# Kernel tuning notes

Measured on AMD Instinct MI355X. Metric: run time of the kernel, lower is better.

Reference implementation:

```python
import jax, jax.numpy as jnp
import numpy as np

V, E, H, N, L = 32000, 512, 512, 64, 128


def setup_inputs() -> dict:
    key = jax.random.key(0)
    ks = jax.random.split(key, 16)
    s = 0.02  # init scale
    return {
        "input_ids": jax.random.randint(ks[0], (N,), 0, V),
        "h": jax.random.normal(ks[1], (N, H), jnp.float32),
        "c": jax.random.normal(ks[2], (N, H), jnp.float32),
        "encoder_hiddens": jax.random.normal(ks[3], (N, L, H), jnp.float32),
        "attn_mask": jnp.zeros((N, L), dtype=bool),
        "embed_W": jax.random.normal(ks[4], (V, E), jnp.float32) * s,
        "w_ih": jax.random.normal(ks[5], (4 * H, E), jnp.float32) * s,
        "b_ih": jnp.zeros((4 * H,), jnp.float32),
        "w_hh": jax.random.normal(ks[6], (4 * H, H), jnp.float32) * s,
        "b_hh": jnp.zeros((4 * H,), jnp.float32),
        "attn_Wh": jax.random.normal(ks[7], (H, H), jnp.float32) * s,
        "attn_Ws": jax.random.normal(ks[8], (H, H), jnp.float32) * s,
        "attn_v": jax.random.normal(ks[9], (H,), jnp.float32) * s,
        "h2o_W": jax.random.normal(ks[10], (V, 2 * H), jnp.float32) * s,
        "h2o_b": jnp.zeros((V,), jnp.float32),
    }


def reference(input_ids, h, c, encoder_hiddens, attn_mask, embed_W,
              w_ih, b_ih, w_hh, b_hh, attn_Wh, attn_Ws, attn_v,
              h2o_W, h2o_b):
    # Embedding lookup: (N, E)
    emb = embed_W[input_ids]
    # LSTM cell: fused gate GEMMs, chunk order i, f, g, o (torch chunk(4))
    gates = emb @ w_ih.T + b_ih + h @ w_hh.T + b_hh  # (N, 4H)
    i_g, f_g, g_g, o_g = jnp.split(gates, 4, axis=1)
    c_t = jax.nn.sigmoid(f_g) * c + jax.nn.sigmoid(i_g) * jnp.tanh(g_g)
    h_t = jax.nn.sigmoid(o_g) * jnp.tanh(c_t)  # (N, H)
    # Bahdanau attention: v^T tanh(W_h h_t + W_s enc)
    proj = jnp.tanh((h_t @ attn_Wh.T)[:, None, :] + encoder_hiddens @ attn_Ws.T)  # (N, L, H)
    score = jnp.einsum('nlh,h->nl', proj, attn_v)  # (N, L)
    score = jnp.where(attn_mask, -jnp.inf, score)
    attn_w = jax.nn.softmax(score, axis=1)  # (N, L)
    context = jnp.einsum('nl,nlh->nh', attn_w, encoder_hiddens)  # (N, H)
    # Output projection + log-softmax over vocab
    combined = jnp.concatenate([h_t, context], axis=1)  # (N, 2H)
    out = jax.nn.log_softmax(combined @ h2o_W.T + h2o_b, axis=-1)  # (N, V)
    return out, h_t, c_t
```

## Files before the change

### kernel.cpp

```cpp
#include <hip/hip_runtime.h>
#include <math.h>

#define V 32000
#define E 512
#define H 512
#define N 64
#define L 128
#define NV (N*V)
#define NH (N*H)
#define MTOT (N*L)
#define VT 500

typedef short  s8v  __attribute__((ext_vector_type(8)));
typedef float  f4v  __attribute__((ext_vector_type(4)));

__device__ __forceinline__ float sigf(float x) { return 1.0f / (1.0f + __expf(-x)); }

__device__ __forceinline__ unsigned short f2bf(float f) {
    unsigned int u = __float_as_uint(f);
    unsigned int r = u + 0x7FFFu + ((u >> 16) & 1u);
    return (unsigned short)(r >> 16);
}

__global__ __launch_bounds__(256) void k_gates(
    const int* __restrict__ ids, const float* __restrict__ hprev,
    const float* __restrict__ embW, const float* __restrict__ w_ih,
    const float* __restrict__ w_hh, float* __restrict__ gates_p)
{
    __shared__ __align__(16) float xs[64 * 128];
    const int bx = blockIdx.x;
    const int ks = blockIdx.y;
    const int tid = threadIdx.x;
    const bool emb_part = (ks < 4);
    const int koff = (ks & 3) * 128;

    for (int i = tid; i < 64 * 32; i += 256) {
        int n = i >> 5, kk4 = i & 31;
        float4 x4;
        if (emb_part)
            x4 = ((const float4*)(embW + (size_t)ids[n] * E + koff))[kk4];
        else
            x4 = ((const float4*)(hprev + (size_t)n * H + koff))[kk4];
        ((float4*)xs)[n * 32 + kk4] = x4;
    }
    __syncthreads();

    const int jl = tid & 63;
    const int ng = tid >> 6;
    const int j = bx * 64 + jl;
    const int nb = ng * 16;
    const float* wrow = (emb_part ? w_ih : w_hh) + (size_t)j * 512 + koff;

    float acc[16];
#pragma unroll
    for (int i = 0; i < 16; ++i) acc[i] = 0.f;

    for (int e4 = 0; e4 < 32; ++e4) {
        float4 w4 = ((const float4*)wrow)[e4];
#pragma unroll
        for (int i = 0; i < 16; ++i) {
            float4 x4 = ((const float4*)xs)[(nb + i) * 32 + e4];
            acc[i] += w4.x * x4.x + w4.y * x4.y + w4.z * x4.z + w4.w * x4.w;
        }
    }
#pragma unroll
    for (int i = 0; i < 16; ++i)
        gates_p[(size_t)ks * (64 * 2048) + (size_t)(nb + i) * 2048 + j] = acc[i];
}

__global__ __launch_bounds__(256) void k_lstm_pw(
    const float* __restrict__ gates_p, const float* __restrict__ b_ih,
    const float* __restrict__ b_hh, const float* __restrict__ cprev,
    float* __restrict__ out, unsigned short* __restrict__ xb)
{
    int i = blockIdx.x * 256 + threadIdx.x;
    if (i >= NH) return;
    int n = i >> 9, k = i & 511;
    float g[4];
#pragma unroll
    for (int q = 0; q < 4; ++q) {
        int j = q * 512 + k;
        float s = b_ih[j] + b_hh[j];
#pragma unroll
        for (int ks = 0; ks < 8; ++ks)
            s += gates_p[(size_t)ks * (64 * 2048) + (size_t)n * 2048 + j];
        g[q] = s;
    }
    float ig = sigf(g[0]), fg = sigf(g[1]), gg = tanhf(g[2]), og = sigf(g[3]);
    float ct = fg * cprev[i] + ig * gg;
    float ht = og * tanhf(ct);
    out[NV + i] = ht;
    out[NV + NH + i] = ct;
    xb[(size_t)n * 1024 + k] = f2bf(ht);
}

__global__ __launch_bounds__(256) void k_sproj(
    const float* __restrict__ out, const float* __restrict__ Wh,
    float* __restrict__ sproj)
{
    __shared__ __align__(16) float xs[512];
    int n = blockIdx.x >> 1;
    int h = (blockIdx.x & 1) * 256 + threadIdx.x;
    const float* ht = out + NV + (size_t)n * 512;
    for (int i = threadIdx.x; i < 512; i += 256) xs[i] = ht[i];
    __syncthreads();
    const float* wrow = Wh + (size_t)h * 512;
    float acc = 0.f;
    for (int e4 = 0; e4 < 128; ++e4) {
        float4 w4 = ((const float4*)wrow)[e4];
        float4 x4 = ((const float4*)xs)[e4];
        acc += w4.x * x4.x + w4.y * x4.y + w4.z * x4.z + w4.w * x4.w;
    }
    sproj[(size_t)n * 512 + h] = acc;
}

__global__ __launch_bounds__(256) void k_score_gemm(
    const float* __restrict__ enc, const float* __restrict__ Ws,
    const float* __restrict__ sproj, const float* __restrict__ av,
    float* __restrict__ scorep)
{
    __shared__ __align__(16) short As[64 * 72];
    __shared__ __align__(16) short Bs[64 * 72];
    __shared__ float sred[64];

    const int bm = blockIdx.x, bh = blockIdx.y;
    const int tid = threadIdx.x;
    const int w = tid >> 6, l = tid & 63;
    const int wave_m = (w >> 1) * 32, wave_h = (w & 1) * 32;
    const int lq = l >> 4, lr = l & 15;

    if (tid < 64) sred[tid] = 0.f;

    f4v acc[2][2];
#pragma unroll
    for (int i = 0; i < 2; ++i)
#pragma unroll
        for (int j = 0; j < 2; ++j) acc[i][j] = (f4v)0.f;

    for (int kt = 0; kt < 8; ++kt) {
        __syncthreads();
#pragma unroll
        for (int r = 0; r < 2; ++r) {
            int idx = (r * 256 + tid) * 8;
            int row = idx >> 6, col = idx & 63;
            const float* sa = enc + (size_t)(bm * 64 + row) * 512 + kt * 64 + col;
            const float* sb = Ws  + (size_t)(bh * 64 + row) * 512 + kt * 64 + col;
            float4 a0 = *(const float4*)sa, a1 = *(const float4*)(sa + 4);
            float4 b0 = *(const float4*)sb, b1 = *(const float4*)(sb + 4);
            union { unsigned short u[8]; uint4 q; } pa, pb;
            pa.u[0]=f2bf(a0.x); pa.u[1]=f2bf(a0.y); pa.u[2]=f2bf(a0.z); pa.u[3]=f2bf(a0.w);
            pa.u[4]=f2bf(a1.x); pa.u[5]=f2bf(a1.y); pa.u[6]=f2bf(a1.z); pa.u[7]=f2bf(a1.w);
            pb.u[0]=f2bf(b0.x); pb.u[1]=f2bf(b0.y); pb.u[2]=f2bf(b0.z); pb.u[3]=f2bf(b0.w);
            pb.u[4]=f2bf(b1.x); pb.u[5]=f2bf(b1.y); pb.u[6]=f2bf(b1.z); pb.u[7]=f2bf(b1.w);
            *(uint4*)(As + row * 72 + col) = pa.q;
            *(uint4*)(Bs + row * 72 + col) = pb.q;
        }
        __syncthreads();

#pragma unroll
        for (int ks = 0; ks < 2; ++ks) {
            s8v a_frag[2], b_frag[2];
#pragma unroll
            for (int i = 0; i < 2; ++i)
                a_frag[i] = *(const s8v*)(As + (wave_m + 16 * i + lr) * 72 + ks * 32 + lq * 8);
#pragma unroll
            for (int j = 0; j < 2; ++j)
                b_frag[j] = *(const s8v*)(Bs + (wave_h + 16 * j + lr) * 72 + ks * 32 + lq * 8);
#pragma unroll
            for (int i = 0; i < 2; ++i)
#pragma unroll
                for (int j = 0; j < 2; ++j)
                    acc[i][j] = __builtin_amdgcn_mfma_f32_16x16x32_bf16(
                        a_frag[i], b_frag[j], acc[i][j], 0, 0, 0);
        }
    }
    __syncthreads();

    const int hc0 = bh * 64 + wave_h + lr;
#pragma unroll
    for (int i = 0; i < 2; ++i) {
#pragma unroll
        for (int reg = 0; reg < 4; ++reg) {
            int m_local = wave_m + 16 * i + lq * 4 + reg;
            int m = bm * 64 + m_local;
            int n = m >> 7;
            float p = 0.f;
#pragma unroll
            for (int j = 0; j < 2; ++j) {
                int hc = hc0 + 16 * j;
                float val = acc[i][j][reg] + sproj[(size_t)n * 512 + hc];
                p += tanhf(val) * av[hc];
            }
            p += __shfl_xor(p, 1, 64);
            p += __shfl_xor(p, 2, 64);
            p += __shfl_xor(p, 4, 64);
            p += __shfl_xor(p, 8, 64);
            if (lr == 0) atomicAdd(&sred[m_local], p);
        }
    }
    __syncthreads();
    if (tid < 64)
        scorep[(size_t)bh * MTOT + bm * 64 + tid] = sred[tid];
}

__global__ __launch_bounds__(512) void k_softmax_ctx(
    const float* __restrict__ scorep, const unsigned char* __restrict__ mask,
    const float* __restrict__ enc, unsigned short* __restrict__ xb)
{
    __shared__ float sc[128];
    __shared__ float wl[128];
    const int n = blockIdx.x, t = threadIdx.x;

    if (t < 128) {
        float s = 0.f;
#pragma unroll
        for (int q = 0; q < 8; ++q)
            s += scorep[(size_t)q * MTOT + n * 128 + t];
        if (mask[(size_t)n * 128 + t]) s = -1e30f;
        sc[t] = s;
    }
    __syncthreads();
    if (t < 64) {
        float m = fmaxf(sc[t], sc[t + 64]);
#pragma unroll
        for (int off = 32; off > 0; off >>= 1) m = fmaxf(m, __shfl_xor(m, off, 64));
        float e0 = __expf(sc[t] - m), e1 = __expf(sc[t + 64] - m);
        float ss = e0 + e1;
#pragma unroll
        for (int off = 32; off > 0; off >>= 1) ss += __shfl_xor(ss, off, 64);
        float inv = 1.0f / ss;
        wl[t] = e0 * inv;
        wl[t + 64] = e1 * inv;
    }
    __syncthreads();

    const float* encn = enc + (size_t)n * L * H + t;
    float acc = 0.f;
#pragma unroll 4
    for (int ll = 0; ll < 128; ++ll)
        acc += wl[ll] * encn[(size_t)ll * 512];
    xb[(size_t)n * 1024 + 512 + t] = f2bf(acc);
}

__global__ __launch_bounds__(256) void k_logits(
    const float* __restrict__ h2oW, const unsigned short* __restrict__ xb,
    const float* __restrict__ h2ob, float* __restrict__ dlogits,
    float* __restrict__ pmax, float* __restrict__ psum)
{
    __shared__ __align__(16) short As[64 * 72];
    __shared__ __align__(16) short Bs[64 * 72];
    __shared__ __align__(16) float cs[64 * 68];

    const int bm = blockIdx.x;
    const int tid = threadIdx.x;
    const int w = tid >> 6, l = tid & 63;
    const int wave_m = (w & 1) * 32, wave_n = (w >> 1) * 32;
    const int lq = l >> 4, lr = l & 15;

    const int arow = tid >> 2;
    const int acol = (tid & 3) * 16;
    const float* aptr = h2oW + (size_t)(bm * 64 + arow) * 1024 + acol;
    const unsigned short* bptr = xb + (size_t)arow * 1024 + acol;

    f4v acc[2][2];
#pragma unroll
    for (int i = 0; i < 2; ++i)
#pragma unroll
        for (int j = 0; j < 2; ++j) acc[i][j] = (f4v)0.f;

    float4 ra[4];
    uint4  rb[2];
#pragma unroll
    for (int r = 0; r < 4; ++r) ra[r] = ((const float4*)aptr)[r];
    rb[0] = *(const uint4*)bptr;
    rb[1] = *(const uint4*)(bptr + 8);

#pragma unroll 1
    for (int kt = 0; kt < 16; ++kt) {
        if (kt) __syncthreads();
        union { unsigned short u[8]; uint4 q; } p0, p1;
        p0.u[0]=f2bf(ra[0].x); p0.u[1]=f2bf(ra[0].y); p0.u[2]=f2bf(ra[0].z); p0.u[3]=f2bf(ra[0].w);
        p0.u[4]=f2bf(ra[1].x); p0.u[5]=f2bf(ra[1].y); p0.u[6]=f2bf(ra[1].z); p0.u[7]=f2bf(ra[1].w);
        p1.u[0]=f2bf(ra[2].x); p1.u[1]=f2bf(ra[2].y); p1.u[2]=f2bf(ra[2].z); p1.u[3]=f2bf(ra[2].w);
        p1.u[4]=f2bf(ra[3].x); p1.u[5]=f2bf(ra[3].y); p1.u[6]=f2bf(ra[3].z); p1.u[7]=f2bf(ra[3].w);
        *(uint4*)(As + arow * 72 + acol)     = p0.q;
        *(uint4*)(As + arow * 72 + acol + 8) = p1.q;
        *(uint4*)(Bs + arow * 72 + acol)     = rb[0];
        *(uint4*)(Bs + arow * 72 + acol + 8) = rb[1];
        __syncthreads();

        if (kt < 15) {
            const float* ap = aptr + (kt + 1) * 64;
            const unsigned short* bp = bptr + (kt + 1) * 64;
#pragma unroll
            for (int r = 0; r < 4; ++r) ra[r] = ((const float4*)ap)[r];
            rb[0] = *(const uint4*)bp;
            rb[1] = *(const uint4*)(bp + 8);
        }

#pragma unroll
        for (int ks = 0; ks < 2; ++ks) {
            s8v a_frag[2], b_frag[2];
#pragma unroll
            for (int i = 0; i < 2; ++i)
                a_frag[i] = *(const s8v*)(As + (wave_m + 16 * i + lr) * 72 + ks * 32 + lq * 8);
#pragma unroll
            for (int j = 0; j < 2; ++j)
                b_frag[j] = *(const s8v*)(Bs + (wave_n + 16 * j + lr) * 72 + ks * 32 + lq * 8);
#pragma unroll
            for (int i = 0; i < 2; ++i)
#pragma unroll
                for (int j = 0; j < 2; ++j)
                    acc[i][j] = __builtin_amdgcn_mfma_f32_16x16x32_bf16(
                        a_frag[i], b_frag[j], acc[i][j], 0, 0, 0);
        }
    }
    __syncthreads();

#pragma unroll
    for (int i = 0; i < 2; ++i)
#pragma unroll
        for (int j = 0; j < 2; ++j)
#pragma unroll
            for (int reg = 0; reg < 4; ++reg)
                cs[(wave_n + 16 * j + lr) * 68 + wave_m + 16 * i + lq * 4 + reg] = acc[i][j][reg];
    __syncthreads();

    const int n = tid >> 2, q = tid & 3;
    const int v0 = bm * 64 + q * 16;
    float4 vals[4];
    float m_loc = -1e30f;
#pragma unroll
    for (int k = 0; k < 4; ++k) {
        float4 cv = *(const float4*)(cs + n * 68 + q * 16 + 4 * k);
        float4 bv = *(const float4*)(h2ob + v0 + 4 * k);
        cv.x += bv.x; cv.y += bv.y; cv.z += bv.z; cv.w += bv.w;
        vals[k] = cv;
        *(float4*)(dlogits + (size_t)n * V + v0 + 4 * k) = cv;
        m_loc = fmaxf(m_loc, fmaxf(fmaxf(cv.x, cv.y), fmaxf(cv.z, cv.w)));
    }
    float s_loc = 0.f;
#pragma unroll
    for (int k = 0; k < 4; ++k) {
        s_loc += __expf(vals[k].x - m_loc) + __expf(vals[k].y - m_loc)
               + __expf(vals[k].z - m_loc) + __expf(vals[k].w - m_loc);
    }
    float m2 = fmaxf(m_loc, __shfl_xor(m_loc, 1, 64));
    m2 = fmaxf(m2, __shfl_xor(m2, 2, 64));
    s_loc *= __expf(m_loc - m2);
    float s2 = s_loc + __shfl_xor(s_loc, 1, 64);
    s2 += __shfl_xor(s2, 2, 64);
    if (q == 0) {
        pmax[(size_t)n * VT + bm] = m2;
        psum[(size_t)n * VT + bm] = s2;
    }
}

__global__ __launch_bounds__(256) void k_lse(
    const float* __restrict__ pmax, const float* __restrict__ psum,
    float* __restrict__ lse)
{
    __shared__ float rm[4], rs[4];
    const int n = blockIdx.x, t = threadIdx.x;
    float m0 = (t < VT) ? pmax[(size_t)n * VT + t] : -1e30f;
    float m1 = (t + 256 < VT) ? pmax[(size_t)n * VT + t + 256] : -1e30f;
    float mm = fmaxf(m0, m1);
#pragma unroll
    for (int off = 32; off > 0; off >>= 1) mm = fmaxf(mm, __shfl_xor(mm, off, 64));
    if ((t & 63) == 0) rm[t >> 6] = mm;
    __syncthreads();
    float m = fmaxf(fmaxf(rm[0], rm[1]), fmaxf(rm[2], rm[3]));

    float s = 0.f;
    if (t < VT)       s += psum[(size_t)n * VT + t] * __expf(m0 - m);
    if (t + 256 < VT) s += psum[(size_t)n * VT + t + 256] * __expf(m1 - m);
#pragma unroll
    for (int off = 32; off > 0; off >>= 1) s += __shfl_xor(s, off, 64);
    if ((t & 63) == 0) rs[t >> 6] = s;
    __syncthreads();
    if (t == 0) {
        float st = rs[0] + rs[1] + rs[2] + rs[3];
        lse[n] = m + __logf(st);
    }
}

__global__ __launch_bounds__(256) void k_norm(
    float* __restrict__ dlogits, const float* __restrict__ lse)
{
    const int n = blockIdx.y;
    const int t4 = blockIdx.x * 256 + threadIdx.x;
    if (t4 >= V / 4) return;
    float s = lse[n];
    float4* p = (float4*)(dlogits + (size_t)n * V) + t4;
    float4 v = *p;
    v.x -= s; v.y -= s; v.z -= s; v.w -= s;
    *p = v;
}

extern "C" void kernel_launch(void* const* d_in, const int* in_sizes, int n_in,
                              void* d_out, int out_size, void* d_ws, size_t ws_size,
                              hipStream_t stream)
{
    const int* ids   = (const int*)d_in[0];
    const float* h   = (const float*)d_in[1];
    const float* c   = (const float*)d_in[2];
    const float* enc = (const float*)d_in[3];
    const unsigned char* mask = (const unsigned char*)d_in[4];
    const float* embW = (const float*)d_in[5];
    const float* w_ih = (const float*)d_in[6];
    const float* b_ih = (const float*)d_in[7];
    const float* w_hh = (const float*)d_in[8];
    const float* b_hh = (const float*)d_in[9];
    const float* Wh   = (const float*)d_in[10];
    const float* Ws   = (const float*)d_in[11];
    const float* av   = (const float*)d_in[12];
    const float* h2oW = (const float*)d_in[13];
    const float* h2ob = (const float*)d_in[14];

    float* out = (float*)d_out;
    float* ws = (float*)d_ws;
    float* gates_p = ws;
    float* sproj   = ws + 1048576;
    float* scorep  = ws + 1048576 + 32768;
    unsigned short* xb = (unsigned short*)(ws + 1048576 + 32768 + 65536);
    float* pmax = ws;
    float* psum = ws + 32000;
    float* lse  = ws + 64000;

    k_gates<<<dim3(32, 8), 256, 0, stream>>>(ids, h, embW, w_ih, w_hh, gates_p);
    k_lstm_pw<<<128, 256, 0, stream>>>(gates_p, b_ih, b_hh, c, out, xb);
    k_sproj<<<128, 256, 0, stream>>>(out, Wh, sproj);
    k_score_gemm<<<dim3(128, 8), 256, 0, stream>>>(enc, Ws, sproj, av, scorep);
    k_softmax_ctx<<<64, 512, 0, stream>>>(scorep, mask, enc, xb);
    k_logits<<<VT, 256, 0, stream>>>(h2oW, xb, h2ob, out, pmax, psum);
    k_lse<<<64, 256, 0, stream>>>(pmax, psum, lse);
    k_norm<<<dim3(32, 64), 256, 0, stream>>>(out, lse);
}
```

Before: 348.9 us.

## Load MFMA fragments directly from global memory, bypassing LDS staging

In the score GEMM and logits GEMM, each lane now loads its own MFMA operand fragments straight from global memory into registers. It converts them with packed bf16 conversions, which removes the shared-memory staging tiles and the block barriers per k-step. The context-softmax kernel is also split into 4 column blocks of 128 threads per batch row to raise parallelism. The tradeoff is that operands loaded once per block are now fetched redundantly across waves through the caches, with less coalescing, and the softmax is recomputed four times per row.

```diff
diff --git a/kernel.cpp b/kernel.cpp
--- a/kernel.cpp
+++ b/kernel.cpp
@@ -1,4 +1,5 @@
 #include <hip/hip_runtime.h>
+#include <hip/hip_bf16.h>
 #include <math.h>
 
 #define V 32000
@@ -22,6 +23,26 @@
     return (unsigned short)(r >> 16);
 }
 
+__device__ __forceinline__ unsigned int cvt2bf(float x, float y) {
+    __hip_bfloat162 h2 = __float22bfloat162_rn(make_float2(x, y));
+    unsigned int r;
+    __builtin_memcpy(&r, &h2, 4);
+    return r;
+}
+
+__device__ __forceinline__ s8v pack_bf8(float4 lo, float4 hi) {
+    union { unsigned int u[4]; s8v s; } r;
+    r.u[0] = cvt2bf(lo.x, lo.y);
+    r.u[1] = cvt2bf(lo.z, lo.w);
+    r.u[2] = cvt2bf(hi.x, hi.y);
+    r.u[3] = cvt2bf(hi.z, hi.w);
+    return r.s;
+}
+
+__device__ __forceinline__ s8v as_s8v(uint4 q) {
+    union { uint4 q; s8v s; } u; u.q = q; return u.s;
+}
+
 __global__ __launch_bounds__(256) void k_gates(
     const int* __restrict__ ids, const float* __restrict__ hprev,
     const float* __restrict__ embW, const float* __restrict__ w_ih,
@@ -119,8 +140,6 @@
     const float* __restrict__ sproj, const float* __restrict__ av,
     float* __restrict__ scorep)
 {
-    __shared__ __align__(16) short As[64 * 72];
-    __shared__ __align__(16) short Bs[64 * 72];
     __shared__ float sred[64];
 
     const int bm = blockIdx.x, bh = blockIdx.y;
@@ -131,48 +150,62 @@
 
     if (tid < 64) sred[tid] = 0.f;
 
+    const float* aP[2];
+    aP[0] = enc + (size_t)(bm * 64 + wave_m + lr) * 512 + lq * 8;
+    aP[1] = aP[0] + 16 * 512;
+    const float* bP[2];
+    bP[0] = Ws + (size_t)(bh * 64 + wave_h + lr) * 512 + lq * 8;
+    bP[1] = bP[0] + 16 * 512;
+
     f4v acc[2][2];
 #pragma unroll
     for (int i = 0; i < 2; ++i)
 #pragma unroll
         for (int j = 0; j < 2; ++j) acc[i][j] = (f4v)0.f;
 
+    float4 ra[2][2][2], rb[2][2][2];
+#pragma unroll
+    for (int i = 0; i < 2; ++i)
+#pragma unroll
+        for (int ks = 0; ks < 2; ++ks) {
+            ra[i][ks][0] = *(const float4*)(aP[i] + ks * 32);
+            ra[i][ks][1] = *(const float4*)(aP[i] + ks * 32 + 4);
+            rb[i][ks][0] = *(const float4*)(bP[i] + ks * 32);
+            rb[i][ks][1] = *(const float4*)(bP[i] + ks * 32 + 4);
+        }
+
+#pragma unroll 1
     for (int kt = 0; kt < 8; ++kt) {
-        __syncthreads();
-#pragma unroll
-        for (int r = 0; r < 2; ++r) {
-            int idx = (r * 256 + tid) * 8;
-            int row = idx >> 6, col = idx & 63;
-            const float* sa = enc + (size_t)(bm * 64 + row) * 512 + kt * 64 + col;
-            const float* sb = Ws  + (size_t)(bh * 64 + row) * 512 + kt * 64 + col;
-            float4 a0 = *(const float4*)sa, a1 = *(const float4*)(sa + 4);
-            float4 b0 = *(const float4*)sb, b1 = *(const float4*)(sb + 4);
-            union { unsigned short u[8]; uint4 q; } pa, pb;
-            pa.u[0]=f2bf(a0.x); pa.u[1]=f2bf(a0.y); pa.u[2]=f2bf(a0.z); pa.u[3]=f2bf(a0.w);
-            pa.u[4]=f2bf(a1.x); pa.u[5]=f2bf(a1.y); pa.u[6]=f2bf(a1.z); pa.u[7]=f2bf(a1.w);
-            pb.u[0]=f2bf(b0.x); pb.u[1]=f2bf(b0.y); pb.u[2]=f2bf(b0.z); pb.u[3]=f2bf(b0.w);
-            pb.u[4]=f2bf(b1.x); pb.u[5]=f2bf(b1.y); pb.u[6]=f2bf(b1.z); pb.u[7]=f2bf(b1.w);
-            *(uint4*)(As + row * 72 + col) = pa.q;
-            *(uint4*)(Bs + row * 72 + col) = pb.q;
-        }
-        __syncthreads();
-
-#pragma unroll
-        for (int ks = 0; ks < 2; ++ks) {
-            s8v a_frag[2], b_frag[2];
+        s8v a_frag[2][2], b_frag[2][2];
+#pragma unroll
+        for (int i = 0; i < 2; ++i)
+#pragma unroll
+            for (int ks = 0; ks < 2; ++ks) {
+                a_frag[i][ks] = pack_bf8(ra[i][ks][0], ra[i][ks][1]);
+                b_frag[i][ks] = pack_bf8(rb[i][ks][0], rb[i][ks][1]);
+            }
+
+        if (kt < 7) {
+            const int off = (kt + 1) * 64;
 #pragma unroll
             for (int i = 0; i < 2; ++i)
-                a_frag[i] = *(const s8v*)(As + (wave_m + 16 * i + lr) * 72 + ks * 32 + lq * 8);
-#pragma unroll
-            for (int j = 0; j < 2; ++j)
-                b_frag[j] = *(const s8v*)(Bs + (wave_h + 16 * j + lr) * 72 + ks * 32 + lq * 8);
+#pragma unroll
+                for (int ks = 0; ks < 2; ++ks) {
+                    ra[i][ks][0] = *(const float4*)(aP[i] + off + ks * 32);
+                    ra[i][ks][1] = *(const float4*)(aP[i] + off + ks * 32 + 4);
+                    rb[i][ks][0] = *(const float4*)(bP[i] + off + ks * 32);
+                    rb[i][ks][1] = *(const float4*)(bP[i] + off + ks * 32 + 4);
+                }
+        }
+
+#pragma unroll
+        for (int ks = 0; ks < 2; ++ks)
 #pragma unroll
             for (int i = 0; i < 2; ++i)
 #pragma unroll
                 for (int j = 0; j < 2; ++j)
                     acc[i][j] = __builtin_amdgcn_mfma_f32_16x16x32_bf16(
-                        a_frag[i], b_frag[j], acc[i][j], 0, 0, 0);
-        }
+                        a_frag[i][ks], b_frag[j][ks], acc[i][j], 0, 0, 0);
     }
     __syncthreads();
 
@@ -203,43 +236,42 @@
         scorep[(size_t)bh * MTOT + bm * 64 + tid] = sred[tid];
 }
 
-__global__ __launch_bounds__(512) void k_softmax_ctx(
+__global__ __launch_bounds__(128) void k_softmax_ctx(
     const float* __restrict__ scorep, const unsigned char* __restrict__ mask,
     const float* __restrict__ enc, unsigned short* __restrict__ xb)
 {
-    __shared__ float sc[128];
     __shared__ float wl[128];
-    const int n = blockIdx.x, t = threadIdx.x;
-
-    if (t < 128) {
-        float s = 0.f;
-#pragma unroll
-        for (int q = 0; q < 8; ++q)
-            s += scorep[(size_t)q * MTOT + n * 128 + t];
-        if (mask[(size_t)n * 128 + t]) s = -1e30f;
-        sc[t] = s;
-    }
-    __syncthreads();
-    if (t < 64) {
-        float m = fmaxf(sc[t], sc[t + 64]);
-#pragma unroll
-        for (int off = 32; off > 0; off >>= 1) m = fmaxf(m, __shfl_xor(m, off, 64));
-        float e0 = __expf(sc[t] - m), e1 = __expf(sc[t + 64] - m);
-        float ss = e0 + e1;
-#pragma unroll
-        for (int off = 32; off > 0; off >>= 1) ss += __shfl_xor(ss, off, 64);
-        float inv = 1.0f / ss;
-        wl[t] = e0 * inv;
-        wl[t + 64] = e1 * inv;
-    }
-    __syncthreads();
-
-    const float* encn = enc + (size_t)n * L * H + t;
+    __shared__ float red[4];
+    const int n = blockIdx.x, hc = blockIdx.y, t = threadIdx.x;
+
+    float s = 0.f;
+#pragma unroll
+    for (int q = 0; q < 8; ++q)
+        s += scorep[(size_t)q * MTOT + n * 128 + t];
+    if (mask[(size_t)n * 128 + t]) s = -1e30f;
+
+    float m = s;
+#pragma unroll
+    for (int off = 32; off > 0; off >>= 1) m = fmaxf(m, __shfl_xor(m, off, 64));
+    if ((t & 63) == 0) red[t >> 6] = m;
+    __syncthreads();
+    m = fmaxf(red[0], red[1]);
+    float e = __expf(s - m);
+    float ss = e;
+#pragma unroll
+    for (int off = 32; off > 0; off >>= 1) ss += __shfl_xor(ss, off, 64);
+    if ((t & 63) == 0) red[2 + (t >> 6)] = ss;
+    __syncthreads();
+    float inv = 1.0f / (red[2] + red[3]);
+    wl[t] = e * inv;
+    __syncthreads();
+
+    const float* encn = enc + (size_t)n * (L * H) + hc * 128 + t;
     float acc = 0.f;
 #pragma unroll 4
     for (int ll = 0; ll < 128; ++ll)
         acc += wl[ll] * encn[(size_t)ll * 512];
-    xb[(size_t)n * 1024 + 512 + t] = f2bf(acc);
+    xb[(size_t)n * 1024 + 512 + hc * 128 + t] = f2bf(acc);
 }
 
 __global__ __launch_bounds__(256) void k_logits(
@@ -247,8 +279,6 @@
     const float* __restrict__ h2ob, float* __restrict__ dlogits,
     float* __restrict__ pmax, float* __restrict__ psum)
 {
-    __shared__ __align__(16) short As[64 * 72];
-    __shared__ __align__(16) short Bs[64 * 72];
     __shared__ __align__(16) float cs[64 * 68];
 
     const int bm = blockIdx.x;
@@ -257,10 +287,12 @@
     const int wave_m = (w & 1) * 32, wave_n = (w >> 1) * 32;
     const int lq = l >> 4, lr = l & 15;
 
-    const int arow = tid >> 2;
-    const int acol = (tid & 3) * 16;
-    const float* aptr = h2oW + (size_t)(bm * 64 + arow) * 1024 + acol;
-    const unsigned short* bptr = xb + (size_t)arow * 1024 + acol;
+    const float* aP[2];
+    aP[0] = h2oW + (size_t)(bm * 64 + wave_m + lr) * 1024 + lq * 8;
+    aP[1] = aP[0] + 16 * 1024;
+    const unsigned short* bP[2];
+    bP[0] = xb + (size_t)(wave_n + lr) * 1024 + lq * 8;
+    bP[1] = bP[0] + 16 * 1024;
 
     f4v acc[2][2];
 #pragma unroll
@@ -268,54 +300,60 @@
 #pragma unroll
         for (int j = 0; j < 2; ++j) acc[i][j] = (f4v)0.f;
 
-    float4 ra[4];
-    uint4  rb[2];
-#pragma unroll
-    for (int r = 0; r < 4; ++r) ra[r] = ((const float4*)aptr)[r];
-    rb[0] = *(const uint4*)bptr;
-    rb[1] = *(const uint4*)(bptr + 8);
+    float4 ra[2][2][2];
+    uint4  rb[2][2];
+#pragma unroll
+    for (int i = 0; i < 2; ++i)
+#pragma unroll
+        for (int ks = 0; ks < 2; ++ks) {
+            ra[i][ks][0] = *(const float4*)(aP[i] + ks * 32);
+            ra[i][ks][1] = *(const float4*)(aP[i] + ks * 32 + 4);
+        }
+#pragma unroll
+    for (int j = 0; j < 2; ++j)
+#pragma unroll
+        for (int ks = 0; ks < 2; ++ks)
+            rb[j][ks] = *(const uint4*)(bP[j] + ks * 32);
 
 #pragma unroll 1
     for (int kt = 0; kt < 16; ++kt) {
-        if (kt) __syncthreads();
-        union { unsigned short u[8]; uint4 q; } p0, p1;
-        p0.u[0]=f2bf(ra[0].x); p0.u[1]=f2bf(ra[0].y); p0.u[2]=f2bf(ra[0].z); p0.u[3]=f2bf(ra[0].w);
-        p0.u[4]=f2bf(ra[1].x); p0.u[5]=f2bf(ra[1].y); p0.u[6]=f2bf(ra[1].z); p0.u[7]=f2bf(ra[1].w);
-        p1.u[0]=f2bf(ra[2].x); p1.u[1]=f2bf(ra[2].y); p1.u[2]=f2bf(ra[2].z); p1.u[3]=f2bf(ra[2].w);
-        p1.u[4]=f2bf(ra[3].x); p1.u[5]=f2bf(ra[3].y); p1.u[6]=f2bf(ra[3].z); p1.u[7]=f2bf(ra[3].w);
-        *(uint4*)(As + arow * 72 + acol)     = p0.q;
-        *(uint4*)(As + arow * 72 + acol + 8) = p1.q;
-        *(uint4*)(Bs + arow * 72 + acol)     = rb[0];
-        *(uint4*)(Bs + arow * 72 + acol + 8) = rb[1];
-        __syncthreads();
+        s8v a_frag[2][2], b_frag[2][2];
+#pragma unroll
+        for (int i = 0; i < 2; ++i)
+#pragma unroll
+            for (int ks = 0; ks < 2; ++ks)
+                a_frag[i][ks] = pack_bf8(ra[i][ks][0], ra[i][ks][1]);
+#pragma unroll
+        for (int j = 0; j < 2; ++j)
+#pragma unroll
+            for (int ks = 0; ks < 2; ++ks)
+                b_frag[j][ks] = as_s8v(rb[j][ks]);
 
         if (kt < 15) {
-            const float* ap = aptr + (kt + 1) * 64;
-            const unsigned short* bp = bptr + (kt + 1) * 64;
-#pragma unroll
-            for (int r = 0; r < 4; ++r) ra[r] = ((const float4*)ap)[r];
-            rb[0] = *(const uint4*)bp;
-            rb[1] = *(const uint4*)(bp + 8);
-        }
-
-#pragma unroll
-        for (int ks = 0; ks < 2; ++ks) {
-            s8v a_frag[2], b_frag[2];
+            const int off = (kt + 1) * 64;
 #pragma unroll
             for (int i = 0; i < 2; ++i)
-                a_frag[i] = *(const s8v*)(As + (wave_m + 16 * i + lr) * 72 + ks * 32 + lq * 8);
+#pragma unroll
+                for (int ks = 0; ks < 2; ++ks) {
+                    ra[i][ks][0] = *(const float4*)(aP[i] + off + ks * 32);
+                    ra[i][ks][1] = *(const float4*)(aP[i] + off + ks * 32 + 4);
+                }
 #pragma unroll
             for (int j = 0; j < 2; ++j)
-                b_frag[j] = *(const s8v*)(Bs + (wave_n + 16 * j + lr) * 72 + ks * 32 + lq * 8);
+#pragma unroll
+                for (int ks = 0; ks < 2; ++ks)
+                    rb[j][ks] = *(const uint4*)(bP[j] + off + ks * 32);
+        }
+
+#pragma unroll
+        for (int ks = 0; ks < 2; ++ks)
 #pragma unroll
             for (int i = 0; i < 2; ++i)
 #pragma unroll
                 for (int j = 0; j < 2; ++j)
                     acc[i][j] = __builtin_amdgcn_mfma_f32_16x16x32_bf16(
-                        a_frag[i], b_frag[j], acc[i][j], 0, 0, 0);
-        }
-    }
-    __syncthreads();
+                        a_frag[i][ks], b_frag[j][ks], acc[i][j], 0, 0, 0);
+    }
 
 #pragma unroll
     for (int i = 0; i < 2; ++i)
@@ -431,7 +469,7 @@
     k_lstm_pw<<<128, 256, 0, stream>>>(gates_p, b_ih, b_hh, c, out, xb);
     k_sproj<<<128, 256, 0, stream>>>(out, Wh, sproj);
     k_score_gemm<<<dim3(128, 8), 256, 0, stream>>>(enc, Ws, sproj, av, scorep);
-    k_softmax_ctx<<<64, 512, 0, stream>>>(scorep, mask, enc, xb);
+    k_softmax_ctx<<<dim3(64, 4), 128, 0, stream>>>(scorep, mask, enc, xb);
     k_logits<<<VT, 256, 0, stream>>>(h2oW, xb, h2ob, out, pmax, psum);
     k_lse<<<64, 256, 0, stream>>>(pmax, psum, lse);
     k_norm<<<dim3(32, 64), 256, 0, stream>>>(out, lse);
```

Result: slower. 381.8 us (+9.4%).
